# Kernel tuning notes

Hardware: AMD Instinct MI355X
Metric: run time of the kernel (lower is better)

Reference implementation:

```python
import jax, jax.numpy as jnp
import numpy as np

NEG_INF = float("-inf")
WINDOW = 5  # window_size in LocalAttention; half = WINDOW // 2 = 2


def setup_inputs() -> dict:
    key = jax.random.key(0)
    kq, kk, kv = jax.random.split(key, 3)
    B, L, H, E = 4, 2048, 8, 64
    queries = jax.random.normal(kq, (B, L, H, E), dtype=jnp.float32)
    keys = jax.random.normal(kk, (B, L, H, E), dtype=jnp.float32)
    values = jax.random.normal(kv, (B, L, H, E), dtype=jnp.float32)
    return {"queries": queries, "keys": keys, "values": values}


def reference(queries, keys, values):
    # queries/keys/values: [B, L, H, E]; dropout is identity (eval mode).
    B, L, H, E = queries.shape
    scale = 1.0 / jnp.sqrt(jnp.asarray(E, dtype=queries.dtype))
    # Shared scores for both branches: [B, H, L, S]
    scores = jnp.einsum("blhe,bshe->bhls", queries, keys)

    # Global (unmasked) branch
    A_global = jax.nn.softmax(scale * scores, axis=-1)

    # Local branch: torch mask allows j in [max(i-2,0), min(i+2,L)) => i-2 <= j <= i+1
    half = WINDOW // 2
    i = jnp.arange(L)[:, None]
    j = jnp.arange(L)[None, :]
    allowed = (j - i >= -half) & (j - i < half)  # [L, L], asymmetric window
    local_scores = jnp.where(allowed, scores, NEG_INF)
    A_local = jax.nn.softmax(scale * local_scores, axis=-1)

    # Sum of the two attention outputs == (A_global + A_local) @ V
    out = jnp.einsum("bhls,bshd->blhd", A_global + A_local, values)
    return out
```

## Files before the change

kernel.cpp:

```cpp
#include <hip/hip_runtime.h>
#include <hip/hip_bf16.h>
#include <stdint.h>


#define LQ 2048
#define HQ 8
#define EQ 64
#define BQ 4
#define BN 64
#define RS (HQ * EQ)
#define SCALE_LOG2E 0.18033688011112042f
#define NTILE (LQ / BN)
#define TILE_U32 2048
#define IMG_U32 (BQ * HQ * NTILE * TILE_U32)
#define BMQ 64

typedef __attribute__((ext_vector_type(8))) short bf16x8;
typedef __attribute__((ext_vector_type(4))) float f32x4;
typedef __attribute__((ext_vector_type(4))) unsigned int u32x4;
typedef __attribute__((ext_vector_type(2))) unsigned int u32x2;

static __device__ __forceinline__ unsigned int f2bf(float f) {
    union { float f; unsigned int u; } c; c.f = f;
    return (c.u + 0x8000u) >> 16;
}
static __device__ __forceinline__ unsigned int pk2(float lo, float hi) {
    union { float f; unsigned int u; } a, b; a.f = lo; b.f = hi;
    return ((a.u + 0x8000u) >> 16) | ((b.u + 0x8000u) & 0xffff0000u);
}
static __device__ __forceinline__ float fexp2(float x) {
    float r;
    asm volatile("v_exp_f32 %0, %1\n\ts_nop 1" : "=v"(r) : "v"(x));
    return r;
}
static __device__ __forceinline__ void gload16(const uint32_t* g, void* l) {
    __builtin_amdgcn_global_load_lds(
        (const __attribute__((address_space(1))) unsigned int*)g,
        (__attribute__((address_space(3))) unsigned int*)l, 16, 0, 0);
}

__global__ __launch_bounds__(256) void prepack_kernel(
    const float* __restrict__ K, const float* __restrict__ V,
    uint32_t* __restrict__ Kimg, uint32_t* __restrict__ Vimg)
{
    __shared__ unsigned short vt[64 * 72];

    const int tid = threadIdx.x;
    const int jc  = blockIdx.x;
    const int bh  = blockIdx.y;
    const int b   = bh >> 3;
    const int h   = bh & 7;
    const int j0  = jc * BN;
    const float* Kbh = K + (size_t)b * LQ * RS + h * EQ;
    const float* Vbh = V + (size_t)b * LQ * RS + h * EQ;
    uint32_t* Kt = Kimg + (size_t)(bh * NTILE + jc) * TILE_U32;
    uint32_t* Vt = Vimg + (size_t)(bh * NTILE + jc) * TILE_U32;

    #pragma unroll
    for (int it = 0; it < 2; ++it) {
        int t2 = tid + it * 256;
        int jr = t2 >> 3, eo = t2 & 7;
        const float* src = Kbh + (size_t)(j0 + jr) * RS + eo * 8;
        float4 a  = *(const float4*)src;
        float4 bv = *(const float4*)(src + 4);
        u32x4 p;
        p.x = pk2(a.x, a.y);   p.y = pk2(a.z, a.w);
        p.z = pk2(bv.x, bv.y); p.w = pk2(bv.z, bv.w);
        *(u32x4*)&Kt[jr * 32 + ((eo ^ (jr & 7)) << 2)] = p;
    }

    {
        const int jr = tid >> 2;
        const int e0 = (tid & 3) * 16;
        const float* src = Vbh + (size_t)(j0 + jr) * RS + e0;
        #pragma unroll
        for (int q = 0; q < 4; ++q) {
            float4 a = *(const float4*)(src + q * 4);
            const int e = e0 + q * 4;
            vt[(e + 0) * 72 + jr] = (unsigned short)f2bf(a.x);
            vt[(e + 1) * 72 + jr] = (unsigned short)f2bf(a.y);
            vt[(e + 2) * 72 + jr] = (unsigned short)f2bf(a.z);
            vt[(e + 3) * 72 + jr] = (unsigned short)f2bf(a.w);
        }
    }
    __syncthreads();

    #pragma unroll
    for (int it = 0; it < 2; ++it) {
        const int i  = tid + it * 256;
        const int e  = i >> 3, jo = i & 7;
        u32x4 p = *(const u32x4*)&vt[e * 72 + jo * 8];
        *(u32x4*)&Vt[e * 32 + ((jo ^ (e & 7)) << 2)] = p;
    }
}

__global__ __launch_bounds__(256, 4) void hybrid_attn_v12(
    const float* __restrict__ Q, const float* __restrict__ K,
    const float* __restrict__ V, const uint32_t* __restrict__ Kimg,
    const uint32_t* __restrict__ Vimg, float* __restrict__ O)
{
    __shared__ unsigned short KV[8192];
    __shared__ unsigned short Pt[4][1024];
    __shared__ float sloc[BMQ][4];

    const int tid  = threadIdx.x;
    const int wave = tid >> 6;
    const int lane = tid & 63;
    const int c    = lane & 15;
    const int g    = lane >> 4;
    const int id   = blockIdx.x;
    const int bh   = (id & 7) * 4 + ((id >> 3) & 3);
    const int qt   = id >> 5;
    const int b    = bh >> 3;
    const int h    = bh & 7;
    const int i0   = qt * BMQ;
    const int c7   = c & 7;
    const int sw3  = c7 << 1;

    const float* Qbh = Q + (size_t)b * LQ * RS + h * EQ;
    const float* Kbh = K + (size_t)b * LQ * RS + h * EQ;
    const float* Vbh = V + (size_t)b * LQ * RS + h * EQ;
    float*       Obh = O + (size_t)b * LQ * RS + h * EQ;

    bf16x8 qf[2];
    {
        const int iq = i0 + wave * 16 + c;
        const float* qrow = Qbh + (size_t)iq * RS + g * 8;
        #pragma unroll
        for (int f = 0; f < 2; ++f) {
            float4 a  = *(const float4*)(qrow + f * 32);
            float4 bv = *(const float4*)(qrow + f * 32 + 4);
            union { bf16x8 v; unsigned int u[4]; } fr;
            fr.u[0] = pk2(a.x  * SCALE_LOG2E, a.y  * SCALE_LOG2E);
            fr.u[1] = pk2(a.z  * SCALE_LOG2E, a.w  * SCALE_LOG2E);
            fr.u[2] = pk2(bv.x * SCALE_LOG2E, bv.y * SCALE_LOG2E);
            fr.u[3] = pk2(bv.z * SCALE_LOG2E, bv.w * SCALE_LOG2E);
            qf[f] = fr.v;
        }
    }

    const int fo0 = c * 64 + ((g ^ c7) << 3);
    const int fo1 = c * 64 + (((4 | g) ^ c7) << 3);

    unsigned short* pw[4];
    #pragma unroll
    for (int n = 0; n < 4; ++n)
        pw[n] = &Pt[wave][c * 64 + ((((n << 2) | g) ^ sw3) << 2)];
    unsigned short* pr0 = &Pt[wave][c * 64 + (((g << 1) ^ sw3) << 2)];
    unsigned short* pr1 = &Pt[wave][c * 64 + (((8 | (g << 1)) ^ sw3) << 2)];

    const uint32_t* kgb = Kimg + (size_t)bh * (NTILE * TILE_U32) + wave * 512 + lane * 4;
    const uint32_t* vgb = Vimg + (size_t)bh * (NTILE * TILE_U32) + wave * 512 + lane * 4;

    f32x4 oacc[4];
    #pragma unroll
    for (int eg = 0; eg < 4; ++eg) oacc[eg] = (f32x4){0.f, 0.f, 0.f, 0.f};
    float lsum = 0.f;

    for (int jc = 0; jc < NTILE; ++jc) {
        __syncthreads();
        const uint32_t* kg = kgb + (size_t)jc * TILE_U32;
        const uint32_t* vg = vgb + (size_t)jc * TILE_U32;
        gload16(kg,       &KV[wave * 1024]);
        gload16(kg + 256, &KV[wave * 1024 + 512]);
        gload16(vg,       &KV[4096 + wave * 1024]);
        gload16(vg + 256, &KV[4096 + wave * 1024 + 512]);
        __syncthreads();

        bf16x8 kfr[4][2];
        #pragma unroll
        for (int n = 0; n < 4; ++n) {
            kfr[n][0] = *(const bf16x8*)&KV[n * 1024 + fo0];
            kfr[n][1] = *(const bf16x8*)&KV[n * 1024 + fo1];
        }

        f32x4 sf[4];
        #pragma unroll
        for (int n = 0; n < 4; ++n) {
            f32x4 acc = (f32x4){0.f, 0.f, 0.f, 0.f};
            acc = __builtin_amdgcn_mfma_f32_16x16x32_bf16(kfr[n][0], qf[0], acc, 0, 0, 0);
            acc = __builtin_amdgcn_mfma_f32_16x16x32_bf16(kfr[n][1], qf[1], acc, 0, 0, 0);
            sf[n] = acc;
        }
        float ls = 0.f;
        #pragma unroll
        for (int n = 0; n < 4; ++n) {
            float p0 = fexp2(sf[n][0]);
            float p1 = fexp2(sf[n][1]);
            float p2 = fexp2(sf[n][2]);
            float p3 = fexp2(sf[n][3]);
            ls += (p0 + p1) + (p2 + p3);
            u32x2 pkd;
            pkd.x = pk2(p0, p1);
            pkd.y = pk2(p2, p3);
            *(u32x2*)pw[n] = pkd;
        }
        lsum += ls;
        asm volatile("s_waitcnt lgkmcnt(0)" ::: "memory");

        bf16x8 pf0 = *(const bf16x8*)pr0;
        bf16x8 pf1 = *(const bf16x8*)pr1;
        #pragma unroll
        for (int eg = 0; eg < 4; ++eg) {
            bf16x8 v0 = *(const bf16x8*)&KV[4096 + eg * 1024 + fo0];
            bf16x8 v1 = *(const bf16x8*)&KV[4096 + eg * 1024 + fo1];
            oacc[eg] = __builtin_amdgcn_mfma_f32_16x16x32_bf16(v0, pf0, oacc[eg], 0, 0, 0);
            oacc[eg] = __builtin_amdgcn_mfma_f32_16x16x32_bf16(v1, pf1, oacc[eg], 0, 0, 0);
        }
    }

    float linv;
    {
        float l = lsum;
        l += __shfl_xor(l, 16);
        l += __shfl_xor(l, 32);
        linv = 1.0f / l;
    }

    {
        const int br = tid >> 2;
        const int jj = tid & 3;
        const int i  = i0 + br;
        const int j  = i - 2 + jj;
        float s = -INFINITY;
        if (j >= 0 && j < LQ) {
            const float* qrow = Qbh + (size_t)i * RS;
            const float* krow = Kbh + (size_t)j * RS;
            float acc = 0.f;
            #pragma unroll
            for (int e = 0; e < 64; e += 4) {
                float4 qa = *(const float4*)(qrow + e);
                float4 ka = *(const float4*)(krow + e);
                acc = fmaf(qa.x, ka.x, acc); acc = fmaf(qa.y, ka.y, acc);
                acc = fmaf(qa.z, ka.z, acc); acc = fmaf(qa.w, ka.w, acc);
            }
            s = 0.125f * acc;
        }
        sloc[br][jj] = s;
    }
    __syncthreads();

    {
        const int row = wave * 16 + c;
        const int i   = i0 + row;
        float s0 = sloc[row][0], s1 = sloc[row][1], s2 = sloc[row][2], s3 = sloc[row][3];
        float mx = fmaxf(fmaxf(s0, s1), fmaxf(s2, s3));
        float w0 = expf(s0 - mx), w1 = expf(s1 - mx);
        float w2 = expf(s2 - mx), w3 = expf(s3 - mx);
        float inv = 1.0f / (w0 + w1 + w2 + w3);
        w0 *= inv; w1 *= inv; w2 *= inv; w3 *= inv;
        const float li = linv;
        float* orow = Obh + (size_t)i * RS;
        #pragma unroll
        for (int eg = 0; eg < 4; ++eg) {
            const int e0 = eg * 16 + g * 4;
            float v0 = oacc[eg][0] * li;
            float v1 = oacc[eg][1] * li;
            float v2 = oacc[eg][2] * li;
            float v3 = oacc[eg][3] * li;
            if (w0 > 0.f) {
                float4 vv = *(const float4*)(Vbh + (size_t)(i - 2) * RS + e0);
                v0 = fmaf(w0, vv.x, v0); v1 = fmaf(w0, vv.y, v1);
                v2 = fmaf(w0, vv.z, v2); v3 = fmaf(w0, vv.w, v3);
            }
            if (w1 > 0.f) {
                float4 vv = *(const float4*)(Vbh + (size_t)(i - 1) * RS + e0);
                v0 = fmaf(w1, vv.x, v0); v1 = fmaf(w1, vv.y, v1);
                v2 = fmaf(w1, vv.z, v2); v3 = fmaf(w1, vv.w, v3);
            }
            {
                float4 vv = *(const float4*)(Vbh + (size_t)i * RS + e0);
                v0 = fmaf(w2, vv.x, v0); v1 = fmaf(w2, vv.y, v1);
                v2 = fmaf(w2, vv.z, v2); v3 = fmaf(w2, vv.w, v3);
            }
            if (w3 > 0.f) {
                float4 vv = *(const float4*)(Vbh + (size_t)(i + 1) * RS + e0);
                v0 = fmaf(w3, vv.x, v0); v1 = fmaf(w3, vv.y, v1);
                v2 = fmaf(w3, vv.z, v2); v3 = fmaf(w3, vv.w, v3);
            }
            float4 outv; outv.x = v0; outv.y = v1; outv.z = v2; outv.w = v3;
            *(float4*)(orow + e0) = outv;
        }
    }
}

__global__ __launch_bounds__(256) void hybrid_attn_fb(
    const float* __restrict__ Q, const float* __restrict__ K,
    const float* __restrict__ V, float* __restrict__ O)
{
    __shared__ unsigned short Ks[64 * 64];
    __shared__ unsigned short Vt[64 * 64];
    __shared__ unsigned short Ps[4][16 * 64];
    __shared__ float sloc[64][4];

    const int tid  = threadIdx.x;
    const int wave = tid >> 6;
    const int lane = tid & 63;
    const int c    = lane & 15;
    const int g    = lane >> 4;
    const int qt   = blockIdx.x;
    const int bh   = blockIdx.y;
    const int b    = bh >> 3;
    const int h    = bh & 7;
    const int i0   = qt * 64;

    const float* Qbh = Q + (size_t)b * LQ * RS + h * EQ;
    const float* Kbh = K + (size_t)b * LQ * RS + h * EQ;
    const float* Vbh = V + (size_t)b * LQ * RS + h * EQ;
    float*       Obh = O + (size_t)b * LQ * RS + h * EQ;

    bf16x8 qf[2];
    {
        const int iA = i0 + wave * 16 + c;
        const float* qrow = Qbh + (size_t)iA * RS + g * 8;
        #pragma unroll
        for (int f = 0; f < 2; ++f) {
            float4 a  = *(const float4*)(qrow + f * 32);
            float4 bv = *(const float4*)(qrow + f * 32 + 4);
            union { bf16x8 v; unsigned int u[4]; } fr;
            fr.u[0] = pk2(a.x  * SCALE_LOG2E, a.y  * SCALE_LOG2E);
            fr.u[1] = pk2(a.z  * SCALE_LOG2E, a.w  * SCALE_LOG2E);
            fr.u[2] = pk2(bv.x * SCALE_LOG2E, bv.y * SCALE_LOG2E);
            fr.u[3] = pk2(bv.z * SCALE_LOG2E, bv.w * SCALE_LOG2E);
            qf[f] = fr.v;
        }
    }

    int kfo[4][2], vfo[4][2], pfo[2], pso[4][4];
    #pragma unroll
    for (int n = 0; n < 4; ++n)
        #pragma unroll
        for (int f = 0; f < 2; ++f)
            kfo[n][f] = (n * 16 + c) * 64 + ((((f << 2) | g) ^ (c & 7)) << 3);
    #pragma unroll
    for (int eg = 0; eg < 4; ++eg)
        #pragma unroll
        for (int kh = 0; kh < 2; ++kh)
            vfo[eg][kh] = (eg * 16 + c) * 64 + ((((kh << 2) | g) ^ (c & 7)) << 3);
    #pragma unroll
    for (int kh = 0; kh < 2; ++kh)
        pfo[kh] = c * 64 + ((((kh << 2) | g) ^ (c & 7)) << 3);
    #pragma unroll
    for (int r = 0; r < 4; ++r) {
        const int row = g * 4 + r;
        #pragma unroll
        for (int n = 0; n < 4; ++n) {
            const int col = n * 16 + c;
            pso[r][n] = row * 64 + ((((col >> 3) ^ (row & 7)) << 3) | (col & 7));
        }
    }

    f32x4 oacc[4];
    #pragma unroll
    for (int eg = 0; eg < 4; ++eg) oacc[eg] = (f32x4){0.f, 0.f, 0.f, 0.f};
    float l_r[4] = {0.f, 0.f, 0.f, 0.f};

    for (int j0 = 0; j0 < LQ; j0 += BN) {
        __syncthreads();
        #pragma unroll
        for (int it = 0; it < 2; ++it) {
            int t2 = tid + it * 256;
            int jr = t2 >> 3, eo = t2 & 7;
            const float* src = Kbh + (size_t)(j0 + jr) * RS + eo * 8;
            float4 a  = *(const float4*)src;
            float4 bv = *(const float4*)(src + 4);
            u32x4 p;
            p.x = pk2(a.x, a.y);   p.y = pk2(a.z, a.w);
            p.z = pk2(bv.x, bv.y); p.w = pk2(bv.z, bv.w);
            *(u32x4*)&Ks[jr * 64 + ((eo ^ (jr & 7)) << 3)] = p;
        }
        #pragma unroll
        for (int it = 0; it < 2; ++it) {
            int t2 = tid + it * 256;
            int e = t2 & 63, jo = t2 >> 6;
            const float* src = Vbh + (size_t)(j0 + jo * 8) * RS + e;
            float v0 = src[0 * RS], v1 = src[1 * RS], v2 = src[2 * RS], v3 = src[3 * RS];
            float v4 = src[4 * RS], v5 = src[5 * RS], v6 = src[6 * RS], v7 = src[7 * RS];
            u32x4 p;
            p.x = pk2(v0, v1); p.y = pk2(v2, v3);
            p.z = pk2(v4, v5); p.w = pk2(v6, v7);
            *(u32x4*)&Vt[e * 64 + ((jo ^ (e & 7)) << 3)] = p;
        }
        __syncthreads();

        f32x4 sf[4];
        #pragma unroll
        for (int n = 0; n < 4; ++n) {
            bf16x8 k0 = *(const bf16x8*)&Ks[kfo[n][0]];
            bf16x8 k1 = *(const bf16x8*)&Ks[kfo[n][1]];
            f32x4 acc = (f32x4){0.f, 0.f, 0.f, 0.f};
            acc = __builtin_amdgcn_mfma_f32_16x16x32_bf16(qf[0], k0, acc, 0, 0, 0);
            acc = __builtin_amdgcn_mfma_f32_16x16x32_bf16(qf[1], k1, acc, 0, 0, 0);
            sf[n] = acc;
        }
        #pragma unroll
        for (int r = 0; r < 4; ++r) {
            float p0 = fexp2(sf[0][r]);
            float p1 = fexp2(sf[1][r]);
            float p2 = fexp2(sf[2][r]);
            float p3 = fexp2(sf[3][r]);
            l_r[r] += (p0 + p1) + (p2 + p3);
            Ps[wave][pso[r][0]] = (unsigned short)f2bf(p0);
            Ps[wave][pso[r][1]] = (unsigned short)f2bf(p1);
            Ps[wave][pso[r][2]] = (unsigned short)f2bf(p2);
            Ps[wave][pso[r][3]] = (unsigned short)f2bf(p3);
        }
        asm volatile("s_waitcnt lgkmcnt(0)" ::: "memory");

        bf16x8 pf0 = *(const bf16x8*)&Ps[wave][pfo[0]];
        bf16x8 pf1 = *(const bf16x8*)&Ps[wave][pfo[1]];
        #pragma unroll
        for (int eg = 0; eg < 4; ++eg) {
            bf16x8 v0 = *(const bf16x8*)&Vt[vfo[eg][0]];
            bf16x8 v1 = *(const bf16x8*)&Vt[vfo[eg][1]];
            oacc[eg] = __builtin_amdgcn_mfma_f32_16x16x32_bf16(pf0, v0, oacc[eg], 0, 0, 0);
            oacc[eg] = __builtin_amdgcn_mfma_f32_16x16x32_bf16(pf1, v1, oacc[eg], 0, 0, 0);
        }
    }

    #pragma unroll
    for (int r = 0; r < 4; ++r) {
        float l = l_r[r];
        l += __shfl_xor(l, 1);
        l += __shfl_xor(l, 2);
        l += __shfl_xor(l, 4);
        l += __shfl_xor(l, 8);
        l_r[r] = 1.0f / l;
    }

    {
        const int br = tid >> 2;
        const int jj = tid & 3;
        const int i  = i0 + br;
        const int j  = i - 2 + jj;
        float s = -INFINITY;
        if (j >= 0 && j < LQ) {
            const float* qrow = Qbh + (size_t)i * RS;
            const float* krow = Kbh + (size_t)j * RS;
            float acc = 0.f;
            #pragma unroll
            for (int e = 0; e < 64; e += 4) {
                float4 qa = *(const float4*)(qrow + e);
                float4 ka = *(const float4*)(krow + e);
                acc = fmaf(qa.x, ka.x, acc); acc = fmaf(qa.y, ka.y, acc);
                acc = fmaf(qa.z, ka.z, acc); acc = fmaf(qa.w, ka.w, acc);
            }
            s = 0.125f * acc;
        }
        sloc[br][jj] = s;
    }
    __syncthreads();

    #pragma unroll
    for (int r = 0; r < 4; ++r) {
        const int row = wave * 16 + g * 4 + r;
        const int i   = i0 + row;
        float s0 = sloc[row][0], s1 = sloc[row][1], s2 = sloc[row][2], s3 = sloc[row][3];
        float mx = fmaxf(fmaxf(s0, s1), fmaxf(s2, s3));
        float w0 = expf(s0 - mx), w1 = expf(s1 - mx);
        float w2 = expf(s2 - mx), w3 = expf(s3 - mx);
        float inv = 1.0f / (w0 + w1 + w2 + w3);
        w0 *= inv; w1 *= inv; w2 *= inv; w3 *= inv;
        const float li = l_r[r];
        float* orow = Obh + (size_t)i * RS;
        #pragma unroll
        for (int eg = 0; eg < 4; ++eg) {
            const int e = eg * 16 + c;
            float val = oacc[eg][r] * li;
            if (w0 > 0.f) val += w0 * Vbh[(size_t)(i - 2) * RS + e];
            if (w1 > 0.f) val += w1 * Vbh[(size_t)(i - 1) * RS + e];
            if (w2 > 0.f) val += w2 * Vbh[(size_t)(i    ) * RS + e];
            if (w3 > 0.f) val += w3 * Vbh[(size_t)(i + 1) * RS + e];
            orow[e] = val;
        }
    }
}

extern "C" void kernel_launch(void* const* d_in, const int* in_sizes, int n_in,
                              void* d_out, int out_size, void* d_ws, size_t ws_size,
                              hipStream_t stream) {
    (void)in_sizes; (void)n_in; (void)out_size;
    const float* Q = (const float*)d_in[0];
    const float* K = (const float*)d_in[1];
    const float* V = (const float*)d_in[2];
    float* O = (float*)d_out;
    const size_t need = (size_t)2 * IMG_U32 * 4;
    if (ws_size >= need) {
        uint32_t* Kimg = (uint32_t*)d_ws;
        uint32_t* Vimg = Kimg + IMG_U32;
        hipLaunchKernelGGL(prepack_kernel, dim3(NTILE, BQ * HQ), dim3(256), 0, stream,
                           K, V, Kimg, Vimg);
        hipLaunchKernelGGL(hybrid_attn_v12, dim3((LQ / BMQ) * BQ * HQ), dim3(256), 0, stream,
                           Q, K, V, Kimg, Vimg, O);
    } else {
        hipLaunchKernelGGL(hybrid_attn_fb, dim3(LQ / 64, BQ * HQ), dim3(256), 0, stream,
                           Q, K, V, O);
    }
}
```

Measured before the change: 155.5 us.

## Process two K/V tiles per barrier phase and load V through registers

The main loop now stages two 64-key K/V tiles per phase into a doubled shared buffer, which halves the number of block-wide barriers over the sequence. V tiles are fetched with plain global vector loads into registers and then written to shared memory, while K still uses the direct global-to-LDS path. The larger LDS footprint lowers the launch-bounds occupancy hint from 4 to 3 blocks per CU. This may reduce latency hiding across blocks.

```diff
diff --git a/kernel.cpp b/kernel.cpp
--- a/kernel.cpp
+++ b/kernel.cpp
@@ -11,6 +11,7 @@
 #define RS (HQ * EQ)
 #define SCALE_LOG2E 0.18033688011112042f
 #define NTILE (LQ / BN)
+#define NPHASE (NTILE / 2)
 #define TILE_U32 2048
 #define IMG_U32 (BQ * HQ * NTILE * TILE_U32)
 #define BMQ 64
@@ -94,12 +95,12 @@
     }
 }
 
-__global__ __launch_bounds__(256, 4) void hybrid_attn_v12(
+__global__ __launch_bounds__(256, 3) void hybrid_attn_v13(
     const float* __restrict__ Q, const float* __restrict__ K,
     const float* __restrict__ V, const uint32_t* __restrict__ Kimg,
     const uint32_t* __restrict__ Vimg, float* __restrict__ O)
 {
-    __shared__ unsigned short KV[8192];
+    __shared__ unsigned short KV[16384];
     __shared__ unsigned short Pt[4][1024];
     __shared__ float sloc[BMQ][4];
 
@@ -157,55 +158,72 @@
     for (int eg = 0; eg < 4; ++eg) oacc[eg] = (f32x4){0.f, 0.f, 0.f, 0.f};
     float lsum = 0.f;
 
-    for (int jc = 0; jc < NTILE; ++jc) {
+    for (int ph = 0; ph < NPHASE; ++ph) {
         __syncthreads();
-        const uint32_t* kg = kgb + (size_t)jc * TILE_U32;
-        const uint32_t* vg = vgb + (size_t)jc * TILE_U32;
-        gload16(kg,       &KV[wave * 1024]);
-        gload16(kg + 256, &KV[wave * 1024 + 512]);
-        gload16(vg,       &KV[4096 + wave * 1024]);
-        gload16(vg + 256, &KV[4096 + wave * 1024 + 512]);
+
+        u32x4 va[2][2];
+        #pragma unroll
+        for (int t = 0; t < 2; ++t) {
+            const size_t jt = (size_t)(ph * 2 + t) * TILE_U32;
+            const uint32_t* kg = kgb + jt;
+            gload16(kg,       &KV[t * 4096 + wave * 1024]);
+            gload16(kg + 256, &KV[t * 4096 + wave * 1024 + 512]);
+            const uint32_t* vg = vgb + jt;
+            va[t][0] = *(const u32x4*)vg;
+            va[t][1] = *(const u32x4*)(vg + 256);
+        }
+        #pragma unroll
+        for (int t = 0; t < 2; ++t) {
+            *(u32x4*)&KV[8192 + t * 4096 + wave * 1024 + lane * 8]       = va[t][0];
+            *(u32x4*)&KV[8192 + t * 4096 + wave * 1024 + 512 + lane * 8] = va[t][1];
+        }
         __syncthreads();
 
-        bf16x8 kfr[4][2];
-        #pragma unroll
-        for (int n = 0; n < 4; ++n) {
-            kfr[n][0] = *(const bf16x8*)&KV[n * 1024 + fo0];
-            kfr[n][1] = *(const bf16x8*)&KV[n * 1024 + fo1];
-        }
-
-        f32x4 sf[4];
-        #pragma unroll
-        for (int n = 0; n < 4; ++n) {
-            f32x4 acc = (f32x4){0.f, 0.f, 0.f, 0.f};
-            acc = __builtin_amdgcn_mfma_f32_16x16x32_bf16(kfr[n][0], qf[0], acc, 0, 0, 0);
-            acc = __builtin_amdgcn_mfma_f32_16x16x32_bf16(kfr[n][1], qf[1], acc, 0, 0, 0);
-            sf[n] = acc;
-        }
-        float ls = 0.f;
-        #pragma unroll
-        for (int n = 0; n < 4; ++n) {
-            float p0 = fexp2(sf[n][0]);
-            float p1 = fexp2(sf[n][1]);
-            float p2 = fexp2(sf[n][2]);
-            float p3 = fexp2(sf[n][3]);
-            ls += (p0 + p1) + (p2 + p3);
-            u32x2 pkd;
-            pkd.x = pk2(p0, p1);
-            pkd.y = pk2(p2, p3);
-            *(u32x2*)pw[n] = pkd;
-        }
-        lsum += ls;
-        asm volatile("s_waitcnt lgkmcnt(0)" ::: "memory");
-
-        bf16x8 pf0 = *(const bf16x8*)pr0;
-        bf16x8 pf1 = *(const bf16x8*)pr1;
-        #pragma unroll
-        for (int eg = 0; eg < 4; ++eg) {
-            bf16x8 v0 = *(const bf16x8*)&KV[4096 + eg * 1024 + fo0];
-            bf16x8 v1 = *(const bf16x8*)&KV[4096 + eg * 1024 + fo1];
-            oacc[eg] = __builtin_amdgcn_mfma_f32_16x16x32_bf16(v0, pf0, oacc[eg], 0, 0, 0);
-            oacc[eg] = __builtin_amdgcn_mfma_f32_16x16x32_bf16(v1, pf1, oacc[eg], 0, 0, 0);
+        #pragma unroll
+        for (int t = 0; t < 2; ++t) {
+            const int kb = t * 4096;
+            const int vb = 8192 + t * 4096;
+
+            bf16x8 kfr[4][2];
+            #pragma unroll
+            for (int n = 0; n < 4; ++n) {
+                kfr[n][0] = *(const bf16x8*)&KV[kb + n * 1024 + fo0];
+                kfr[n][1] = *(const bf16x8*)&KV[kb + n * 1024 + fo1];
+            }
+
+            f32x4 sf[4];
+            #pragma unroll
+            for (int n = 0; n < 4; ++n) {
+                f32x4 acc = (f32x4){0.f, 0.f, 0.f, 0.f};
+                acc = __builtin_amdgcn_mfma_f32_16x16x32_bf16(kfr[n][0], qf[0], acc, 0, 0, 0);
+                acc = __builtin_amdgcn_mfma_f32_16x16x32_bf16(kfr[n][1], qf[1], acc, 0, 0, 0);
+                sf[n] = acc;
+            }
+            float ls = 0.f;
+            #pragma unroll
+            for (int n = 0; n < 4; ++n) {
+                float p0 = fexp2(sf[n][0]);
+                float p1 = fexp2(sf[n][1]);
+                float p2 = fexp2(sf[n][2]);
+                float p3 = fexp2(sf[n][3]);
+                ls += (p0 + p1) + (p2 + p3);
+                u32x2 pkd;
+                pkd.x = pk2(p0, p1);
+                pkd.y = pk2(p2, p3);
+                *(u32x2*)pw[n] = pkd;
+            }
+            lsum += ls;
+            asm volatile("s_waitcnt lgkmcnt(0)" ::: "memory");
+
+            bf16x8 pf0 = *(const bf16x8*)pr0;
+            bf16x8 pf1 = *(const bf16x8*)pr1;
+            #pragma unroll
+            for (int eg = 0; eg < 4; ++eg) {
+                bf16x8 v0 = *(const bf16x8*)&KV[vb + eg * 1024 + fo0];
+                bf16x8 v1 = *(const bf16x8*)&KV[vb + eg * 1024 + fo1];
+                oacc[eg] = __builtin_amdgcn_mfma_f32_16x16x32_bf16(v0, pf0, oacc[eg], 0, 0, 0);
+                oacc[eg] = __builtin_amdgcn_mfma_f32_16x16x32_bf16(v1, pf1, oacc[eg], 0, 0, 0);
+            }
         }
     }
 
@@ -490,7 +508,7 @@
         uint32_t* Vimg = Kimg + IMG_U32;
         hipLaunchKernelGGL(prepack_kernel, dim3(NTILE, BQ * HQ), dim3(256), 0, stream,
                            K, V, Kimg, Vimg);
-        hipLaunchKernelGGL(hybrid_attn_v12, dim3((LQ / BMQ) * BQ * HQ), dim3(256), 0, stream,
+        hipLaunchKernelGGL(hybrid_attn_v13, dim3((LQ / BMQ) * BQ * HQ), dim3(256), 0, stream,
                            Q, K, V, Kimg, Vimg, O);
     } else {
         hipLaunchKernelGGL(hybrid_attn_fb, dim3(LQ / 64, BQ * HQ), dim3(256), 0, stream,
```

After: 166.1 us. 1.07x slower.
